# Kernel optimization log

Hardware: AMD Instinct MI355X
Metric: run time of the kernel (lower is better)

## Reference

```python
import jax, jax.numpy as jnp
import numpy as np

B, D, T, K = 32, 64, 4096, 512
COMMITMENT_COST = 0.25


def setup_inputs() -> dict:
    key = jax.random.key(0)
    k1, k2 = jax.random.split(key)
    z = jax.random.normal(k1, (B, D, T), dtype=jnp.float32)
    # nn.Embedding init: uniform(-1/K, 1/K)
    codebook = jax.random.uniform(k2, (K, D), dtype=jnp.float32,
                                  minval=-1.0 / K, maxval=1.0 / K)
    return {"z": z, "codebook": codebook}


def reference(z, codebook):
    sg = jax.lax.stop_gradient
    zt = jnp.transpose(z, (0, 2, 1))            # [B, T, D]
    zf = zt.reshape(-1, D)                      # [N, D], N = B*T
    # squared L2 distances: ||z||^2 + ||e||^2 - 2 z.e  -> [N, K]
    dists = (jnp.sum(zf * zf, axis=1, keepdims=True)
             + jnp.sum(codebook * codebook, axis=1)
             - 2.0 * jnp.matmul(zf, codebook.T))
    idx = jnp.argmin(dists, axis=1)             # [N]
    # gather codebook rows (same math as one-hot @ codebook)
    quantized = codebook[idx].reshape(zt.shape)  # [B, T, D]
    codebook_loss = jnp.mean((sg(quantized) - zt) ** 2)
    commitment_loss = jnp.mean((quantized - sg(zt)) ** 2)
    vq_loss = codebook_loss + COMMITMENT_COST * commitment_loss
    # straight-through estimator
    quantized_st = zt + sg(quantized - zt)
    quantized_out = jnp.transpose(quantized_st, (0, 2, 1))  # [B, D, T]
    indices = idx.reshape(B, T)
    return vq_loss, quantized_out, indices
```

## Files before the change

### kernel.cpp

```cpp
#include <hip/hip_runtime.h>

#define NB 32
#define ND 64
#define NT 4096
#define NK 512
#define NGRID 1024

typedef __attribute__((ext_vector_type(8))) short short8;
typedef __attribute__((ext_vector_type(16))) float f32x16;
typedef unsigned int uint32;
typedef unsigned short ushort16_t;

#define PERM(r) ((((r) & 7) * 16) + ((r) >> 3))
#define STR 68
#define ESTR 66
#define M2 2.5e-4f
#define RCAP 4

__device__ __forceinline__ ushort16_t bf16rne(float f) {
    uint32 u = __float_as_uint(f);
    return (ushort16_t)((u + 0x7FFFu + ((u >> 16) & 1u)) >> 16);
}
__device__ __forceinline__ float bf16tof(ushort16_t h) {
    return __uint_as_float(((uint32)h) << 16);
}

__global__ void prep_kernel(const float* __restrict__ cb,
                            uint4* __restrict__ cbfrag,
                            float* __restrict__ enorm,
                            double* __restrict__ loss_acc,
                            uint32* __restrict__ counter) {
    const int bi = blockIdx.x, tid = threadIdx.x;
    if (bi < 16) {
        const int t = bi * 256 + tid;
        const int c = t >> 8, rem = t & 255, s = rem >> 6, L = rem & 63;
        const int kcode = c * 32 + (L & 31);
        const int dbase = s * 16 + ((L >> 5) << 3);
        const float* src = cb + (size_t)kcode * 64 + dbase;
        const float4 pa = *(const float4*)src;
        const float4 pb = *(const float4*)(src + 4);
        const float f[8] = {pa.x, pa.y, pa.z, pa.w, pb.x, pb.y, pb.z, pb.w};
        uint32 hw[4], lw[4];
#pragma unroll
        for (int i = 0; i < 4; ++i) {
            const ushort16_t h0 = bf16rne(f[2*i]);
            const ushort16_t h1 = bf16rne(f[2*i+1]);
            const ushort16_t l0 = bf16rne(f[2*i]   - bf16tof(h0));
            const ushort16_t l1 = bf16rne(f[2*i+1] - bf16tof(h1));
            hw[i] = (uint32)h0 | ((uint32)h1 << 16);
            lw[i] = (uint32)l0 | ((uint32)l1 << 16);
        }
        cbfrag[(size_t)((c*4+s)*2 + 0)*64 + L] = make_uint4(hw[0],hw[1],hw[2],hw[3]);
        cbfrag[(size_t)((c*4+s)*2 + 1)*64 + L] = make_uint4(lw[0],lw[1],lw[2],lw[3]);
    } else {
        if (tid == 0) { *loss_acc = 0.0; *counter = 0u; }
        for (int k = tid; k < NK; k += 256) {
            const float* e = cb + (size_t)k * ND;
            float r[8];
#pragma unroll
            for (int j = 0; j < 8; ++j) {
                float s = __fmul_rn(e[j], e[j]);
#pragma unroll
                for (int i = 1; i < 8; ++i)
                    s = __fadd_rn(s, __fmul_rn(e[8*i+j], e[8*i+j]));
                r[j] = s;
            }
            enorm[k] = __fadd_rn(__fadd_rn(__fadd_rn(r[0],r[1]), __fadd_rn(r[2],r[3])),
                                 __fadd_rn(__fadd_rn(r[4],r[5]), __fadd_rn(r[6],r[7])));
        }
    }
}

__device__ __forceinline__ float exact_dist(const float* __restrict__ zrow,
                                            const float* __restrict__ cb,
                                            const float* __restrict__ enl,
                                            float zn, int k2) {
    const float4* e4 = (const float4*)(cb + (size_t)k2 * ND);
    float a = 0.0f;
#pragma unroll
    for (int w = 0; w < 16; ++w) {
        const float4 ev = e4[w];
        const float4 zv = *(const float4*)(zrow + 4 * w);
        a = __builtin_fmaf(zv.x, ev.x, a);
        a = __builtin_fmaf(zv.y, ev.y, a);
        a = __builtin_fmaf(zv.z, ev.z, a);
        a = __builtin_fmaf(zv.w, ev.w, a);
    }
    return __fsub_rn(__fadd_rn(zn, enl[k2]), __fmul_rn(2.0f, a));
}

__global__ __launch_bounds__(256, 3) void vq_main(const float* __restrict__ z,
                                                  const float* __restrict__ cb,
                                                  const uint4* __restrict__ cbfrag,
                                                  const float* __restrict__ enorm,
                                                  float* __restrict__ qout,
                                                  float* __restrict__ idxout,
                                                  double* __restrict__ loss_acc,
                                                  uint32* __restrict__ counter,
                                                  float* __restrict__ out0) {
    __shared__ __align__(16) char smem[39968];
    float*       zl   = (float*)smem;
    float*       enl  = (float*)(smem + 34816);
    float*       znl  = (float*)(smem + 36864);
    ushort16_t*  cand = (ushort16_t*)(smem + 37376);
    int*         sfin = (int*)(smem + 39424);
    double*      sred = (double*)(smem + 39936);

    const int bi    = blockIdx.x;
    const int b     = bi >> 5;
    const int tbase = (bi & 31) * 128;
    const int tid   = threadIdx.x;
    const size_t zoff = (size_t)b * (ND * NT) + tbase;

#pragma unroll
    for (int j = 0; j < 8; ++j) {
        const int qq = j * 256 + tid;
        const int i4 = qq & 31, d = qq >> 5;
        const float4 v = *(const float4*)(z + zoff + (size_t)d * NT + i4 * 4);
        const float vv[4] = {v.x, v.y, v.z, v.w};
#pragma unroll
        for (int c = 0; c < 4; ++c) {
            const int r = i4 * 4 + c;
            zl[PERM(r) * STR + d] = vv[c];
        }
    }
    for (int k = tid; k < NK; k += 256) enl[k] = enorm[k];
    __syncthreads();

    if (tid < 128) {
        const int r = tid;
        const float4* zr4 = (const float4*)&zl[PERM(r) * STR];
        float x[64];
#pragma unroll
        for (int wq = 0; wq < 16; ++wq) {
            const float4 t4 = zr4[wq];
            x[4*wq] = t4.x; x[4*wq+1] = t4.y; x[4*wq+2] = t4.z; x[4*wq+3] = t4.w;
        }
        float r8[8];
#pragma unroll
        for (int jj = 0; jj < 8; ++jj) {
            float s = __fmul_rn(x[jj], x[jj]);
#pragma unroll
            for (int ii = 1; ii < 8; ++ii)
                s = __fadd_rn(s, __fmul_rn(x[8*ii+jj], x[8*ii+jj]));
            r8[jj] = s;
        }
        znl[r] = __fadd_rn(__fadd_rn(__fadd_rn(r8[0],r8[1]), __fadd_rn(r8[2],r8[3])),
                           __fadd_rn(__fadd_rn(r8[4],r8[5]), __fadd_rn(r8[6],r8[7])));
    }

    const int L    = tid & 63;
    const int w    = tid >> 6;
    const int h    = L >> 5;
    const int rowl = w * 32 + (L & 31);
    short8 bhf[4], blf[4];
    {
        const float* zrow = &zl[PERM(rowl) * STR];
#pragma unroll
        for (int s = 0; s < 4; ++s) {
            const int d0 = s * 16 + h * 8;
            const float4 pa = *(const float4*)(zrow + d0);
            const float4 pb = *(const float4*)(zrow + d0 + 4);
            const float f[8] = {pa.x, pa.y, pa.z, pa.w, pb.x, pb.y, pb.z, pb.w};
            uint32 hw[4], lw[4];
#pragma unroll
            for (int i = 0; i < 4; ++i) {
                const ushort16_t h0 = bf16rne(f[2*i]);
                const ushort16_t h1 = bf16rne(f[2*i+1]);
                const ushort16_t l0 = bf16rne(f[2*i]   - bf16tof(h0));
                const ushort16_t l1 = bf16rne(f[2*i+1] - bf16tof(h1));
                hw[i] = (uint32)h0 | ((uint32)h1 << 16);
                lw[i] = (uint32)l0 | ((uint32)l1 << 16);
            }
            union { uint4 u; short8 s8; } uh, ul;
            uh.u = make_uint4(hw[0],hw[1],hw[2],hw[3]);
            ul.u = make_uint4(lw[0],lw[1],lw[2],lw[3]);
            bhf[s] = uh.s8; blf[s] = ul.s8;
        }
    }
    __syncthreads();

    const int h4 = h * 4;

    uint32 p1 = 0u, p2 = 0u, p3 = 0u;
#pragma unroll 2
    for (int c = 0; c < 16; ++c) {
        uint4 B[8];
#pragma unroll
        for (int p = 0; p < 8; ++p) B[p] = cbfrag[(size_t)((c * 8 + p) * 64) + L];
        f32x16 acc;
#pragma unroll
        for (int r = 0; r < 16; ++r) acc[r] = 0.0f;
#pragma unroll
        for (int s = 0; s < 4; ++s) {
            union { uint4 u; short8 s8; } ah, al;
            ah.u = B[s * 2 + 0];
            al.u = B[s * 2 + 1];
            acc = __builtin_amdgcn_mfma_f32_32x32x16_bf16(ah.s8, bhf[s], acc, 0, 0, 0);
            acc = __builtin_amdgcn_mfma_f32_32x32x16_bf16(al.s8, bhf[s], acc, 0, 0, 0);
            acc = __builtin_amdgcn_mfma_f32_32x32x16_bf16(ah.s8, blf[s], acc, 0, 0, 0);
        }
#pragma unroll
        for (int r = 0; r < 16; ++r) {
            const int kc = c * 32 + ((r & 3) + 8 * (r >> 2)) + h4;
            const uint32 pv = (__float_as_uint(fmaxf(acc[r] + 1.0f, 0.0f)) & ~0x1FFu)
                            | (uint32)kc;
            const bool g1 = pv > p1, g2 = pv > p2, g3 = pv > p3;
            p3 = g2 ? p2 : (g3 ? pv : p3);
            p2 = g1 ? p1 : (g2 ? pv : p2);
            p1 = g1 ? pv : p1;
        }
    }

    const uint32 op1 = __shfl_xor(p1, 32);
    const uint32 pkG = (p1 > op1) ? p1 : op1;
    const int    kG  = (int)(pkG & 0x1FFu);
    {
    }
    const float  bm   = __uint_as_float(pkG & ~0x1FFu) - 1.0f;
    const float  thrf = bm - M2;
    const uint32 thrF = __float_as_uint(fmaxf(thrf + 1.0f, 0.0f)) & ~0x1FFu;

    const float* zrow = &zl[PERM(rowl) * STR];
    const float  zn   = znl[rowl];
    const int    iown = (((kG >> 2) & 1) == h);

    int bkf;
    if (__any((int)(p3 >= thrF))) {
        int myc = 0, ovf = 0;
        ushort16_t* mylist = cand + (rowl * 2 + h) * RCAP;
#pragma unroll 1
        for (int c = 0; c < 16; ++c) {
            uint4 B[8];
#pragma unroll
            for (int p = 0; p < 8; ++p) B[p] = cbfrag[(size_t)((c * 8 + p) * 64) + L];
            f32x16 acc;
#pragma unroll
            for (int r = 0; r < 16; ++r) acc[r] = 0.0f;
#pragma unroll
            for (int s = 0; s < 4; ++s) {
                union { uint4 u; short8 s8; } ah, al;
                ah.u = B[s * 2 + 0];
                al.u = B[s * 2 + 1];
                acc = __builtin_amdgcn_mfma_f32_32x32x16_bf16(ah.s8, bhf[s], acc, 0, 0, 0);
                acc = __builtin_amdgcn_mfma_f32_32x32x16_bf16(al.s8, bhf[s], acc, 0, 0, 0);
                acc = __builtin_amdgcn_mfma_f32_32x32x16_bf16(ah.s8, blf[s], acc, 0, 0, 0);
            }
#pragma unroll
            for (int r = 0; r < 16; ++r) {
                const int kc = c * 32 + ((r & 3) + 8 * (r >> 2)) + h4;
                const uint32 pv = (__float_as_uint(fmaxf(acc[r] + 1.0f, 0.0f)) & ~0x1FFu)
                                | (uint32)kc;
                if (pv >= thrF && kc != kG) {
                    if (myc < RCAP) mylist[myc++] = (ushort16_t)kc;
                    else ovf = 1;
                }
            }
        }
        const int totr = myc + __shfl_xor(myc, 32);
        const int aovf = ovf | __shfl_xor(ovf, 32);
        if (aovf) {
            float bd = __builtin_inff(); bkf = 0x7FFFFFFF;
            for (int c = 0; c < 16; ++c)
#pragma unroll
                for (int qd = 0; qd < 4; ++qd)
#pragma unroll
                    for (int i = 0; i < 4; ++i) {
                        const int k2c = c * 32 + qd * 8 + h * 4 + i;
                        const float dv = exact_dist(zrow, cb, enl, zn, k2c);
                        if (dv < bd || (dv == bd && k2c < bkf)) { bd = dv; bkf = k2c; }
                    }
            const float obd = __shfl_xor(bd, 32);
            const int   obq = __shfl_xor(bkf, 32);
            if (obd < bd || (obd == bd && obq < bkf)) bkf = obq;
        } else if (totr > 0) {
            float bd = __builtin_inff(); bkf = 0x7FFFFFFF;
            if (iown) { bd = exact_dist(zrow, cb, enl, zn, kG); bkf = kG; }
            for (int i = 0; i < myc; ++i) {
                const int k2c = mylist[i];
                const float dv = exact_dist(zrow, cb, enl, zn, k2c);
                if (dv < bd || (dv == bd && k2c < bkf)) { bd = dv; bkf = k2c; }
            }
            const float obd = __shfl_xor(bd, 32);
            const int   obq = __shfl_xor(bkf, 32);
            if (obd < bd || (obd == bd && obq < bkf)) bkf = obq;
        } else {
            bkf = kG;
        }
    } else {
        const int k1 = (int)(p1 & 0x1FFu);
        const int k2 = (int)(p2 & 0x1FFu);
        const int r1v = (!iown) && (p1 >= thrF);
        const int r2v = (p2 >= thrF);
        const int nr  = r1v + r2v;
        const int totr = nr + __shfl_xor(nr, 32);
        if (totr > 0) {
            float bd = __builtin_inff(); bkf = 0x7FFFFFFF;
            if (iown) { bd = exact_dist(zrow, cb, enl, zn, kG); bkf = kG; }
            if (r1v) {
                const float dv = exact_dist(zrow, cb, enl, zn, k1);
                if (dv < bd || (dv == bd && k1 < bkf)) { bd = dv; bkf = k1; }
            }
            if (r2v) {
                const float dv = exact_dist(zrow, cb, enl, zn, k2);
                if (dv < bd || (dv == bd && k2 < bkf)) { bd = dv; bkf = k2; }
            }
            const float obd = __shfl_xor(bd, 32);
            const int   obq = __shfl_xor(bkf, 32);
            if (obd < bd || (obd == bd && obq < bkf)) bkf = obq;
        } else {
            bkf = kG;
        }
    }

    if (h == 0) {
        sfin[rowl] = bkf;
        idxout[(size_t)b * NT + tbase + rowl] = (float)bkf;
    }
    __syncthreads();

    float* ech = zl;
#pragma unroll
    for (int j = 0; j < 8; ++j) {
        const int qq  = j * 256 + tid;
        const int row = qq >> 4, d4 = qq & 15;
        const float4 v = *(const float4*)(cb + (size_t)sfin[row] * ND + d4 * 4);
        float* dst = &ech[row * ESTR + d4 * 4];
        *(float2*)(dst)     = make_float2(v.x, v.y);
        *(float2*)(dst + 2) = make_float2(v.z, v.w);
    }
    __syncthreads();

    double lsum = 0.0;
#pragma unroll 4
    for (int j = 0; j < 32; ++j) {
        const int qq = j * 256 + tid;
        const int ir = qq & 127, d = qq >> 7;
        const float zv = z[zoff + (size_t)d * NT + ir];
        const float ev = ech[ir * ESTR + d];
        const float diff = __fsub_rn(ev, zv);
        qout[(size_t)b * (ND*NT) + (size_t)d * NT + tbase + ir] = __fadd_rn(zv, diff);
        lsum += (double)diff * (double)diff;
    }
#pragma unroll
    for (int off = 32; off > 0; off >>= 1) lsum += __shfl_down(lsum, off, 64);
    if ((tid & 63) == 0) sred[tid >> 6] = lsum;
    __syncthreads();

    if (tid == 0) {
        const double bsum = (sred[0] + sred[1]) + (sred[2] + sred[3]);
        atomicAdd(loss_acc, bsum);
        __threadfence();
        const uint32 old = atomicAdd(counter, 1u);
        if (old == (uint32)(NGRID - 1)) {
            __threadfence();
            const double tot = *(volatile double*)loss_acc;
            const double m = tot / (double)((size_t)NB * NT * ND);
            out0[0] = (float)(1.25 * m);
        }
    }
}

extern "C" void kernel_launch(void* const* d_in, const int* in_sizes, int n_in,
                              void* d_out, int out_size, void* d_ws, size_t ws_size,
                              hipStream_t stream) {
    const float* z  = (const float*)d_in[0];
    const float* cb = (const float*)d_in[1];

    float* out      = (float*)d_out;
    float* loss_out = out;
    float* qout     = out + 1;
    float* idxout   = out + 1 + (size_t)NB * ND * NT;

    uint4*  cbfrag   = (uint4*)d_ws;
    float*  enorm    = (float*)((char*)d_ws + 139264);
    double* loss_acc = (double*)((char*)d_ws + 141312);
    uint32* counter  = (uint32*)((char*)d_ws + 141320);

    prep_kernel<<<17, 256, 0, stream>>>(cb, cbfrag, enorm, loss_acc, counter);
    vq_main<<<NGRID, 256, 0, stream>>>(z, cb, cbfrag, enorm, qout, idxout,
                                       loss_acc, counter, loss_out);
}
```

Measured before the change: 187.4 us.

## Double-buffer codebook fragment loads, compute z-norm lazily, spread loss atomics

Result: faster. 176.1 us (-6.0%).

```diff
diff --git a/kernel.cpp b/kernel.cpp
--- a/kernel.cpp
+++ b/kernel.cpp
@@ -16,6 +16,7 @@
 #define ESTR 66
 #define M2 2.5e-4f
 #define RCAP 4
+#define NSLOT 16
 
 __device__ __forceinline__ ushort16_t bf16rne(float f) {
     uint32 u = __float_as_uint(f);
@@ -53,7 +54,8 @@
         cbfrag[(size_t)((c*4+s)*2 + 0)*64 + L] = make_uint4(hw[0],hw[1],hw[2],hw[3]);
         cbfrag[(size_t)((c*4+s)*2 + 1)*64 + L] = make_uint4(lw[0],lw[1],lw[2],lw[3]);
     } else {
-        if (tid == 0) { *loss_acc = 0.0; *counter = 0u; }
+        if (tid < NSLOT) loss_acc[tid] = 0.0;
+        if (tid == 0) *counter = 0u;
         for (int k = tid; k < NK; k += 256) {
             const float* e = cb + (size_t)k * ND;
             float r[8];
@@ -87,6 +89,25 @@
         a = __builtin_fmaf(zv.w, ev.w, a);
     }
     return __fsub_rn(__fadd_rn(zn, enl[k2]), __fmul_rn(2.0f, a));
+}
+
+__device__ __forceinline__ float znorm_of(const float* __restrict__ zrow) {
+    float r8[8];
+    const float4* zr4 = (const float4*)zrow;
+#pragma unroll
+    for (int wq = 0; wq < 16; ++wq) {
+        const float4 t4 = zr4[wq];
+        const float v[4] = {t4.x, t4.y, t4.z, t4.w};
+#pragma unroll
+        for (int m = 0; m < 4; ++m) {
+            const int f = 4 * wq + m;
+            const int jj = f & 7;
+            if (f < 8) r8[jj] = __fmul_rn(v[m], v[m]);
+            else       r8[jj] = __fadd_rn(r8[jj], __fmul_rn(v[m], v[m]));
+        }
+    }
+    return __fadd_rn(__fadd_rn(__fadd_rn(r8[0],r8[1]), __fadd_rn(r8[2],r8[3])),
+                     __fadd_rn(__fadd_rn(r8[4],r8[5]), __fadd_rn(r8[6],r8[7])));
 }
 
 __global__ __launch_bounds__(256, 3) void vq_main(const float* __restrict__ z,
@@ -98,13 +119,12 @@
                                                   double* __restrict__ loss_acc,
                                                   uint32* __restrict__ counter,
                                                   float* __restrict__ out0) {
-    __shared__ __align__(16) char smem[39968];
+    __shared__ __align__(16) char smem[39456];
     float*       zl   = (float*)smem;
     float*       enl  = (float*)(smem + 34816);
-    float*       znl  = (float*)(smem + 36864);
-    ushort16_t*  cand = (ushort16_t*)(smem + 37376);
-    int*         sfin = (int*)(smem + 39424);
-    double*      sred = (double*)(smem + 39936);
+    ushort16_t*  cand = (ushort16_t*)(smem + 36864);
+    int*         sfin = (int*)(smem + 38912);
+    double*      sred = (double*)(smem + 39424);
 
     const int bi    = blockIdx.x;
     const int b     = bi >> 5;
@@ -126,28 +146,6 @@
     }
     for (int k = tid; k < NK; k += 256) enl[k] = enorm[k];
     __syncthreads();
-
-    if (tid < 128) {
-        const int r = tid;
-        const float4* zr4 = (const float4*)&zl[PERM(r) * STR];
-        float x[64];
-#pragma unroll
-        for (int wq = 0; wq < 16; ++wq) {
-            const float4 t4 = zr4[wq];
-            x[4*wq] = t4.x; x[4*wq+1] = t4.y; x[4*wq+2] = t4.z; x[4*wq+3] = t4.w;
-        }
-        float r8[8];
-#pragma unroll
-        for (int jj = 0; jj < 8; ++jj) {
-            float s = __fmul_rn(x[jj], x[jj]);
-#pragma unroll
-            for (int ii = 1; ii < 8; ++ii)
-                s = __fadd_rn(s, __fmul_rn(x[8*ii+jj], x[8*ii+jj]));
-            r8[jj] = s;
-        }
-        znl[r] = __fadd_rn(__fadd_rn(__fadd_rn(r8[0],r8[1]), __fadd_rn(r8[2],r8[3])),
-                           __fadd_rn(__fadd_rn(r8[4],r8[5]), __fadd_rn(r8[6],r8[7])));
-    }
 
     const int L    = tid & 63;
     const int w    = tid >> 6;
@@ -178,51 +176,54 @@
             bhf[s] = uh.s8; blf[s] = ul.s8;
         }
     }
-    __syncthreads();
 
     const int h4 = h * 4;
 
     uint32 p1 = 0u, p2 = 0u, p3 = 0u;
+    {
+        uint4 buf0[8], buf1[8];
+#pragma unroll
+        for (int p = 0; p < 8; ++p) buf0[p] = cbfrag[(size_t)p * 64 + L];
 #pragma unroll 2
-    for (int c = 0; c < 16; ++c) {
-        uint4 B[8];
-#pragma unroll
-        for (int p = 0; p < 8; ++p) B[p] = cbfrag[(size_t)((c * 8 + p) * 64) + L];
-        f32x16 acc;
-#pragma unroll
-        for (int r = 0; r < 16; ++r) acc[r] = 0.0f;
-#pragma unroll
-        for (int s = 0; s < 4; ++s) {
-            union { uint4 u; short8 s8; } ah, al;
-            ah.u = B[s * 2 + 0];
-            al.u = B[s * 2 + 1];
-            acc = __builtin_amdgcn_mfma_f32_32x32x16_bf16(ah.s8, bhf[s], acc, 0, 0, 0);
-            acc = __builtin_amdgcn_mfma_f32_32x32x16_bf16(al.s8, bhf[s], acc, 0, 0, 0);
-            acc = __builtin_amdgcn_mfma_f32_32x32x16_bf16(ah.s8, blf[s], acc, 0, 0, 0);
-        }
-#pragma unroll
-        for (int r = 0; r < 16; ++r) {
-            const int kc = c * 32 + ((r & 3) + 8 * (r >> 2)) + h4;
-            const uint32 pv = (__float_as_uint(fmaxf(acc[r] + 1.0f, 0.0f)) & ~0x1FFu)
-                            | (uint32)kc;
-            const bool g1 = pv > p1, g2 = pv > p2, g3 = pv > p3;
-            p3 = g2 ? p2 : (g3 ? pv : p3);
-            p2 = g1 ? p1 : (g2 ? pv : p2);
-            p1 = g1 ? pv : p1;
+        for (int c = 0; c < 16; ++c) {
+            const uint4* cur = (c & 1) ? buf1 : buf0;
+            uint4*       nxt = (c & 1) ? buf0 : buf1;
+#pragma unroll
+            for (int p = 0; p < 8; ++p)
+                nxt[p] = cbfrag[(size_t)((c + 1) * 8 + p) * 64 + L];
+            f32x16 acc;
+#pragma unroll
+            for (int r = 0; r < 16; ++r) acc[r] = 0.0f;
+#pragma unroll
+            for (int s = 0; s < 4; ++s) {
+                union { uint4 u; short8 s8; } ah, al;
+                ah.u = cur[s * 2 + 0];
+                al.u = cur[s * 2 + 1];
+                acc = __builtin_amdgcn_mfma_f32_32x32x16_bf16(ah.s8, bhf[s], acc, 0, 0, 0);
+                acc = __builtin_amdgcn_mfma_f32_32x32x16_bf16(al.s8, bhf[s], acc, 0, 0, 0);
+                acc = __builtin_amdgcn_mfma_f32_32x32x16_bf16(ah.s8, blf[s], acc, 0, 0, 0);
+            }
+#pragma unroll
+            for (int r = 0; r < 16; ++r) {
+                const int kc = c * 32 + ((r & 3) + 8 * (r >> 2)) + h4;
+                const uint32 pv = (__float_as_uint(fmaxf(acc[r] + 1.0f, 0.0f)) & ~0x1FFu)
+                                | (uint32)kc;
+                const bool g1 = pv > p1, g2 = pv > p2, g3 = pv > p3;
+                p3 = g2 ? p2 : (g3 ? pv : p3);
+                p2 = g1 ? p1 : (g2 ? pv : p2);
+                p1 = g1 ? pv : p1;
+            }
         }
     }
 
     const uint32 op1 = __shfl_xor(p1, 32);
     const uint32 pkG = (p1 > op1) ? p1 : op1;
     const int    kG  = (int)(pkG & 0x1FFu);
-    {
-    }
     const float  bm   = __uint_as_float(pkG & ~0x1FFu) - 1.0f;
     const float  thrf = bm - M2;
     const uint32 thrF = __float_as_uint(fmaxf(thrf + 1.0f, 0.0f)) & ~0x1FFu;
 
     const float* zrow = &zl[PERM(rowl) * STR];
-    const float  zn   = znl[rowl];
     const int    iown = (((kG >> 2) & 1) == h);
 
     int bkf;
@@ -260,6 +261,7 @@
         const int totr = myc + __shfl_xor(myc, 32);
         const int aovf = ovf | __shfl_xor(ovf, 32);
         if (aovf) {
+            const float zn = znorm_of(zrow);
             float bd = __builtin_inff(); bkf = 0x7FFFFFFF;
             for (int c = 0; c < 16; ++c)
 #pragma unroll
@@ -274,6 +276,7 @@
             const int   obq = __shfl_xor(bkf, 32);
             if (obd < bd || (obd == bd && obq < bkf)) bkf = obq;
         } else if (totr > 0) {
+            const float zn = znorm_of(zrow);
             float bd = __builtin_inff(); bkf = 0x7FFFFFFF;
             if (iown) { bd = exact_dist(zrow, cb, enl, zn, kG); bkf = kG; }
             for (int i = 0; i < myc; ++i) {
@@ -295,6 +298,7 @@
         const int nr  = r1v + r2v;
         const int totr = nr + __shfl_xor(nr, 32);
         if (totr > 0) {
+            const float zn = znorm_of(zrow);
             float bd = __builtin_inff(); bkf = 0x7FFFFFFF;
             if (iown) { bd = exact_dist(zrow, cb, enl, zn, kG); bkf = kG; }
             if (r1v) {
@@ -349,12 +353,14 @@
 
     if (tid == 0) {
         const double bsum = (sred[0] + sred[1]) + (sred[2] + sred[3]);
-        atomicAdd(loss_acc, bsum);
+        atomicAdd(loss_acc + (bi & (NSLOT - 1)), bsum);
         __threadfence();
         const uint32 old = atomicAdd(counter, 1u);
         if (old == (uint32)(NGRID - 1)) {
             __threadfence();
-            const double tot = *(volatile double*)loss_acc;
+            double tot = 0.0;
+            for (int i = 0; i < NSLOT; ++i)
+                tot += ((volatile double*)loss_acc)[i];
             const double m = tot / (double)((size_t)NB * NT * ND);
             out0[0] = (float)(1.25 * m);
         }
@@ -375,7 +381,7 @@
     uint4*  cbfrag   = (uint4*)d_ws;
     float*  enorm    = (float*)((char*)d_ws + 139264);
     double* loss_acc = (double*)((char*)d_ws + 141312);
-    uint32* counter  = (uint32*)((char*)d_ws + 141320);
+    uint32* counter  = (uint32*)((char*)d_ws + 141440);
 
     prep_kernel<<<17, 256, 0, stream>>>(cb, cbfrag, enorm, loss_acc, counter);
     vq_main<<<NGRID, 256, 0, stream>>>(z, cb, cbfrag, enorm, qout, idxout,
```
